# Kernel tuning notes

Hardware: AMD Instinct MI355X
Metric: run time of the kernel (lower is better)

Reference implementation:

```python
import jax, jax.numpy as jnp
import numpy as np

EPS = 1e-5


def setup_inputs() -> dict:
    key = jax.random.key(0)
    k1, k2, k3 = jax.random.split(key, 3)
    B, n_per, C_in, C_out = 8, 131072, 32, 64
    N = B * n_per
    coord = jax.random.uniform(k1, (N, 3), dtype=jnp.float32)          # points in unit cube
    feat = jax.random.normal(k2, (N, C_in), dtype=jnp.float32)
    offset = (jnp.arange(1, B + 1, dtype=jnp.int32) * n_per)           # cumulative counts
    W = jax.random.normal(k3, (C_in, C_out), dtype=jnp.float32) * 0.05  # fc weight (no bias)
    gamma = jnp.ones((C_out,), dtype=jnp.float32)
    beta = jnp.zeros((C_out,), dtype=jnp.float32)
    return {"coord": coord, "feat": feat, "offset": offset, "W": W,
            "gamma": gamma, "beta": beta, "grid_size": 0.05}


def reference(coord, feat, offset, W, gamma, beta, grid_size):
    N = coord.shape[0]
    B = offset.shape[0]
    # offset2batch: point i belongs to batch = first b with i < offset[b]
    batch = jnp.searchsorted(offset, jnp.arange(N, dtype=offset.dtype), side="right").astype(jnp.int32)

    # fc -> BatchNorm (training-mode batch stats, biased var) -> ReLU
    h = feat @ W                                                        # [N, C_out]
    mean = h.mean(axis=0)
    var = jnp.mean((h - mean) ** 2, axis=0)
    h = jax.nn.relu((h - mean) * jax.lax.rsqrt(var + EPS) * gamma + beta)

    # start = per-batch min coord (segment_csr 'min' over batch pointer)
    start = jax.ops.segment_min(coord, batch, num_segments=B)           # [B, 3]

    # voxel_grid: integer voxel coords per point, combined with batch into a unique key
    v = jnp.floor((coord - start[batch]) / grid_size).astype(jnp.int32)  # [N, 3] >= 0
    D = v.max(axis=0) + 1                                               # grid extents
    vkey = ((batch * D[0] + v[:, 0]) * D[1] + v[:, 1]) * D[2] + v[:, 2]

    # unique(sorted) + inverse + counts; then segment mean/max by cluster
    uniq, inverse, counts = jnp.unique(vkey, return_inverse=True, return_counts=True)
    inverse = inverse.reshape(-1).astype(jnp.int32)
    M = uniq.shape[0]
    coord_out = jax.ops.segment_sum(coord, inverse, num_segments=M) / counts[:, None].astype(coord.dtype)
    feat_out = jax.ops.segment_max(h, inverse, num_segments=M)

    # batch id of each cluster (constant within cluster) -> new offset
    batch_out = jax.ops.segment_min(batch, inverse, num_segments=M)
    offset_out = jnp.cumsum(jnp.bincount(batch_out, length=B)).astype(offset.dtype)
    return coord_out, feat_out, offset_out, inverse
```

## Files before the change

kernel.cpp:

```cpp
#include <hip/hip_runtime.h>
#include <float.h>

#define EPSV 1e-5f
#define DGRID 21
#define DPROD (21 * 21 * 21)

typedef __attribute__((ext_vector_type(8))) short bf16x8;
typedef __attribute__((ext_vector_type(4))) float f32x4;

__device__ __forceinline__ short f2bf(float x) {
    unsigned u = __float_as_uint(x);
    unsigned r = (u + 0x7FFFu + ((u >> 16) & 1u)) >> 16;
    return (short)r;
}

__device__ __forceinline__ int batch_of(int i, const int* __restrict__ offset, int B) {
    int b = 0;
    while (b < B - 1 && i >= offset[b]) ++b;
    return b;
}

__global__ void k_init(int* startEnc, int B) {
    int tid = threadIdx.x;
    if (tid < B * 3) startEnc[tid] = 0x7FFFFFFF;
}

__global__ void k_start(const float* __restrict__ coord, const int* __restrict__ offset,
                        int* startEnc, int* counts, int KSM, int N, int B) {
    int gtid = blockIdx.x * blockDim.x + threadIdx.x;
    for (int k = gtid; k < KSM; k += gridDim.x * blockDim.x) counts[k] = 0;

    __shared__ int smin[24];
    int t = threadIdx.x;
    if (t < B * 3) smin[t] = 0x7FFFFFFF;
    __syncthreads();
    int base = gtid * 4;
    int curb = -1;
    int m0 = 0x7FFFFFFF, m1 = 0x7FFFFFFF, m2 = 0x7FFFFFFF;
    for (int r = 0; r < 4; ++r) {
        int i = base + r;
        if (i >= N) break;
        int b = batch_of(i, offset, B);
        if (b != curb) {
            if (curb >= 0) {
                atomicMin(&smin[curb * 3 + 0], m0);
                atomicMin(&smin[curb * 3 + 1], m1);
                atomicMin(&smin[curb * 3 + 2], m2);
            }
            curb = b; m0 = m1 = m2 = 0x7FFFFFFF;
        }
        m0 = min(m0, __float_as_int(coord[(size_t)i * 3 + 0]));
        m1 = min(m1, __float_as_int(coord[(size_t)i * 3 + 1]));
        m2 = min(m2, __float_as_int(coord[(size_t)i * 3 + 2]));
    }
    if (curb >= 0) {
        atomicMin(&smin[curb * 3 + 0], m0);
        atomicMin(&smin[curb * 3 + 1], m1);
        atomicMin(&smin[curb * 3 + 2], m2);
    }
    __syncthreads();
    if (t < B * 3 && smin[t] != 0x7FFFFFFF) atomicMin(&startEnc[t], smin[t]);
}

__global__ void k_count(const float* __restrict__ coord, const int* __restrict__ offset,
                        const int* __restrict__ startEnc, const float* __restrict__ gsP,
                        int* counts, int* vkey, int N, int B) {
    int i = blockIdx.x * blockDim.x + threadIdx.x;
    if (i >= N) return;
    float inv_gs = 1.0f / gsP[0];
    int b = batch_of(i, offset, B);
    float s0 = __int_as_float(startEnc[b * 3 + 0]);
    float s1 = __int_as_float(startEnc[b * 3 + 1]);
    float s2 = __int_as_float(startEnc[b * 3 + 2]);
    int vx = min(DGRID - 1, (int)floorf((coord[(size_t)i * 3 + 0] - s0) * inv_gs));
    int vy = min(DGRID - 1, (int)floorf((coord[(size_t)i * 3 + 1] - s1) * inv_gs));
    int vz = min(DGRID - 1, (int)floorf((coord[(size_t)i * 3 + 2] - s2) * inv_gs));
    int k = ((b * DGRID + vx) * DGRID + vy) * DGRID + vz;
    vkey[i] = k;
    atomicAdd(&counts[k], 1);
}

__global__ void k_scan1(const int* __restrict__ counts, int* occPart, int* cntPart, int KSM) {
    __shared__ int so[256], sc[256];
    int t = threadIdx.x;
    int base = blockIdx.x * 1024 + t * 4;
    int o = 0, c = 0;
    for (int r = 0; r < 4; ++r) {
        int k = base + r;
        if (k < KSM) { int cnt = counts[k]; o += (cnt > 0); c += cnt; }
    }
    so[t] = o; sc[t] = c;
    __syncthreads();
    for (int s = 128; s > 0; s >>= 1) {
        if (t < s) { so[t] += so[t + s]; sc[t] += sc[t + s]; }
        __syncthreads();
    }
    if (t == 0) { occPart[blockIdx.x] = so[0]; cntPart[blockIdx.x] = sc[0]; }
}

__global__ void k_scan2(const int* occPart, const int* cntPart,
                        int* occPartEx, int* cntPartEx, int NBLK) {
    __shared__ int so[128], sc[128];
    int t = threadIdx.x;
    int o = (t < NBLK) ? occPart[t] : 0;
    int c = (t < NBLK) ? cntPart[t] : 0;
    so[t] = o; sc[t] = c;
    __syncthreads();
    for (int s = 1; s < 128; s <<= 1) {
        int ao = 0, ac = 0;
        if (t >= s) { ao = so[t - s]; ac = sc[t - s]; }
        __syncthreads();
        so[t] += ao; sc[t] += ac;
        __syncthreads();
    }
    if (t < NBLK) { occPartEx[t] = so[t] - o; cntPartEx[t] = sc[t] - c; }
}

__global__ void k_scan3(const int* __restrict__ counts, const int* occPartEx, const int* cntPartEx,
                        int* occScan, int* cntScan, int* cursor, int* cntC, int* cstartC, int KSM) {
    __shared__ int so[256], sc[256];
    int t = threadIdx.x;
    int base = blockIdx.x * 1024 + t * 4;
    int o[4], c[4];
    int tO = 0, tC = 0;
    for (int r = 0; r < 4; ++r) {
        int k = base + r;
        int cnt = (k < KSM) ? counts[k] : 0;
        o[r] = (cnt > 0); c[r] = cnt;
        tO += o[r]; tC += c[r];
    }
    so[t] = tO; sc[t] = tC;
    __syncthreads();
    for (int s = 1; s < 256; s <<= 1) {
        int ao = 0, ac = 0;
        if (t >= s) { ao = so[t - s]; ac = sc[t - s]; }
        __syncthreads();
        so[t] += ao; sc[t] += ac;
        __syncthreads();
    }
    int exO = so[t] - tO + occPartEx[blockIdx.x];
    int exC = sc[t] - tC + cntPartEx[blockIdx.x];
    for (int r = 0; r < 4; ++r) {
        int k = base + r;
        if (k < KSM) {
            occScan[k] = exO; cntScan[k] = exC; cursor[k] = 0;
            if (c[r] > 0) { cntC[exO] = c[r]; cstartC[exO] = exC; }
            exO += o[r]; exC += c[r];
        }
    }
}

__global__ void k_scatter(const int* __restrict__ vkey,
                          const int* __restrict__ occScan, const int* __restrict__ cntScan,
                          int* cursor, int* plist, float* __restrict__ dout,
                          int N, int B, int M) {
    int i = blockIdx.x * blockDim.x + threadIdx.x;
    if (i >= N) return;
    int k = vkey[i];
    int cidx = occScan[k];
    int pos = cntScan[k] + atomicAdd(&cursor[k], 1);
    plist[pos] = i;
    dout[(size_t)67 * M + B + i] = (float)cidx;
}

__launch_bounds__(64)
__global__ void k_pool(const float* __restrict__ feat, const float* __restrict__ coord,
                       const float* __restrict__ W,
                       const int* __restrict__ cstartC, const int* __restrict__ cntC,
                       const int* __restrict__ plist,
                       float* __restrict__ dout, float* __restrict__ statPart, int M) {
    const int lane = threadIdx.x;
    const int col  = lane & 15;
    const int quad = lane >> 4;
    const int nw = gridDim.x;
    const int gw = blockIdx.x;

    bf16x8 Bf[4];
#pragma unroll
    for (int t = 0; t < 4; ++t) {
#pragma unroll
        for (int j = 0; j < 8; ++j) {
            int k = quad * 8 + j;
            Bf[t][j] = f2bf(W[k * 64 + t * 16 + col]);
        }
    }

    float sumA[4] = {0.f, 0.f, 0.f, 0.f};
    float sqA[4]  = {0.f, 0.f, 0.f, 0.f};

    for (int c0 = gw; c0 < M; c0 += 2 * nw) {
        int c1 = c0 + nw;
        bool has2 = c1 < M;
        if (!has2) c1 = c0;
        int ps0 = cstartC[c0], n0 = cntC[c0];
        int ps1 = cstartC[c1], n1 = cntC[c1];
        int nmax = max(n0, n1);

        float maxA0[4] = {-FLT_MAX, -FLT_MAX, -FLT_MAX, -FLT_MAX};
        float maxA1[4] = {-FLT_MAX, -FLT_MAX, -FLT_MAX, -FLT_MAX};
        float cacc0 = 0.f, cacc1 = 0.f;

        for (int base = 0; base < nmax; base += 16) {
            int m = base + col;
            int idx0 = min(m, n0 - 1);
            int idx1 = min(m, n1 - 1);
            int p0 = plist[ps0 + idx0];
            int p1 = plist[ps1 + idx1];
            const float4* r0p = reinterpret_cast<const float4*>(feat + (size_t)p0 * 32 + quad * 8);
            const float4* r1p = reinterpret_cast<const float4*>(feat + (size_t)p1 * 32 + quad * 8);
            float4 a00 = r0p[0], a01 = r0p[1];
            float4 a10 = r1p[0], a11 = r1p[1];
            if (quad > 0) {
                float v0 = coord[(size_t)p0 * 3 + (quad - 1)];
                float v1 = coord[(size_t)p1 * 3 + (quad - 1)];
                cacc0 += (m < n0) ? v0 : 0.f;
                cacc1 += (m < n1) ? v1 : 0.f;
            }
            bf16x8 Af0, Af1;
            Af0[0] = f2bf(a00.x); Af0[1] = f2bf(a00.y); Af0[2] = f2bf(a00.z); Af0[3] = f2bf(a00.w);
            Af0[4] = f2bf(a01.x); Af0[5] = f2bf(a01.y); Af0[6] = f2bf(a01.z); Af0[7] = f2bf(a01.w);
            Af1[0] = f2bf(a10.x); Af1[1] = f2bf(a10.y); Af1[2] = f2bf(a10.z); Af1[3] = f2bf(a10.w);
            Af1[4] = f2bf(a11.x); Af1[5] = f2bf(a11.y); Af1[6] = f2bf(a11.z); Af1[7] = f2bf(a11.w);
            f32x4 Cz = {0.f, 0.f, 0.f, 0.f};
#pragma unroll
            for (int t = 0; t < 4; ++t) {
                f32x4 v0 = __builtin_amdgcn_mfma_f32_16x16x32_bf16(Af0, Bf[t], Cz, 0, 0, 0);
                f32x4 v1 = __builtin_amdgcn_mfma_f32_16x16x32_bf16(Af1, Bf[t], Cz, 0, 0, 0);
#pragma unroll
                for (int r = 0; r < 4; ++r) {
                    int rowPt = base + quad * 4 + r;
                    maxA0[t] = fmaxf(maxA0[t], v0[r]);
                    maxA1[t] = fmaxf(maxA1[t], v1[r]);
                    float m0 = (rowPt < n0) ? v0[r] : 0.f;
                    sumA[t] += m0; sqA[t] = fmaf(m0, m0, sqA[t]);
                    float m1 = (rowPt < n1 && has2) ? v1[r] : 0.f;
                    sumA[t] += m1; sqA[t] = fmaf(m1, m1, sqA[t]);
                }
            }
        }
        float out0 = 0.f, out1 = 0.f;
#pragma unroll
        for (int t = 0; t < 4; ++t) {
            float v = maxA0[t];
            v = fmaxf(v, __shfl_xor(v, 16, 64));
            v = fmaxf(v, __shfl_xor(v, 32, 64));
            if (quad == t) out0 = v;
            float w = maxA1[t];
            w = fmaxf(w, __shfl_xor(w, 16, 64));
            w = fmaxf(w, __shfl_xor(w, 32, 64));
            if (quad == t) out1 = w;
        }
        dout[(size_t)3 * M + (size_t)c0 * 64 + lane] = out0;
        dout[(size_t)3 * M + (size_t)c1 * 64 + lane] = out1;

        cacc0 += __shfl_xor(cacc0, 1, 64); cacc0 += __shfl_xor(cacc0, 2, 64);
        cacc0 += __shfl_xor(cacc0, 4, 64); cacc0 += __shfl_xor(cacc0, 8, 64);
        cacc1 += __shfl_xor(cacc1, 1, 64); cacc1 += __shfl_xor(cacc1, 2, 64);
        cacc1 += __shfl_xor(cacc1, 4, 64); cacc1 += __shfl_xor(cacc1, 8, 64);
        if (quad > 0 && col == 0) {
            dout[(size_t)c0 * 3 + (quad - 1)] = cacc0 / (float)n0;
            dout[(size_t)c1 * 3 + (quad - 1)] = cacc1 / (float)n1;
        }
    }

    float so = 0.f, qo = 0.f;
#pragma unroll
    for (int t = 0; t < 4; ++t) {
        float s = sumA[t];
        s += __shfl_xor(s, 16, 64);
        s += __shfl_xor(s, 32, 64);
        float q = sqA[t];
        q += __shfl_xor(q, 16, 64);
        q += __shfl_xor(q, 32, 64);
        if (quad == t) { so = s; qo = q; }
    }
    statPart[(size_t)gw * 128 + lane] = so;
    statPart[(size_t)gw * 128 + 64 + lane] = qo;
}

__global__ void k_statred(const float* __restrict__ statPart,
                          const float* __restrict__ gamma, const float* __restrict__ beta,
                          float* bnA, float* bnB, int NB, int N) {
    __shared__ float s1[256], s2[256];
    int c = blockIdx.x;
    int t = threadIdx.x;
    float a = 0.f, b = 0.f;
    for (int bb = t; bb < NB; bb += 256) {
        a += statPart[(size_t)bb * 128 + c];
        b += statPart[(size_t)bb * 128 + 64 + c];
    }
    s1[t] = a; s2[t] = b;
    __syncthreads();
    for (int s = 128; s > 0; s >>= 1) {
        if (t < s) { s1[t] += s1[t + s]; s2[t] += s2[t + s]; }
        __syncthreads();
    }
    if (t == 0) {
        float invN = 1.0f / (float)N;
        float mean = s1[0] * invN;
        float var = s2[0] * invN - mean * mean;
        float aa = gamma[c] / sqrtf(var + EPSV);
        bnA[c] = aa;
        bnB[c] = beta[c] - mean * aa;
    }
}

__global__ void k_final(float* __restrict__ dout, const float* __restrict__ bnA,
                        const float* __restrict__ bnB,
                        const int* __restrict__ occScan, int M, int B) {
    size_t stride = (size_t)gridDim.x * blockDim.x;
    size_t tid0 = (size_t)blockIdx.x * blockDim.x + threadIdx.x;
    size_t totF = (size_t)M * 64;
    for (size_t t = tid0; t < totF; t += stride) {
        int c = (int)(t & 63);
        float v = dout[(size_t)3 * M + t];
        dout[(size_t)3 * M + t] = fmaxf(bnA[c] * v + bnB[c], 0.f);
    }
    if (tid0 < (size_t)B) {
        int val = (tid0 == (size_t)(B - 1)) ? M : occScan[(int)(tid0 + 1) * DPROD];
        dout[(size_t)67 * M + tid0] = (float)val;
    }
}

extern "C" void kernel_launch(void* const* d_in, const int* in_sizes, int n_in,
                              void* d_out, int out_size, void* d_ws, size_t ws_size,
                              hipStream_t stream) {
    const float* coord = (const float*)d_in[0];
    const float* feat  = (const float*)d_in[1];
    const int*   offset = (const int*)d_in[2];
    const float* W     = (const float*)d_in[3];
    const float* gamma = (const float*)d_in[4];
    const float* beta  = (const float*)d_in[5];
    const float* gsP   = (const float*)d_in[6];
    float* dout = (float*)d_out;

    const int N = in_sizes[0] / 3;
    const int B = in_sizes[2];
    const int M = (out_size - B - N) / 67;
    const int KSM = B * DPROD;
    const int NBLK = (KSM + 1023) / 1024;
    const int NBPL = 8192;

    int* wsI = (int*)d_ws;
    int* startEnc  = wsI + 0;
    float* bnA     = (float*)(wsI + 64);
    float* bnB     = (float*)(wsI + 128);
    int* occPart   = wsI + 256;
    int* cntPart   = wsI + 384;
    int* occPartEx = wsI + 512;
    int* cntPartEx = wsI + 640;
    int* counts    = wsI + 1024;
    int* occScan   = counts + KSM;
    int* cntScan   = occScan + KSM;
    int* cursor    = cntScan + KSM;
    int* cntC      = cursor + KSM;
    int* cstartC   = cntC + KSM;
    int* vkey      = cstartC + KSM;
    int* plist     = vkey + N;
    float* statPart = (float*)(plist + N);

    const int TPB = 256;
    int gChunk = (N + 1023) / 1024;
    int gPoint = (N + TPB - 1) / TPB;

    k_init<<<1, 64, 0, stream>>>(startEnc, B);
    k_start<<<gChunk, TPB, 0, stream>>>(coord, offset, startEnc, counts, KSM, N, B);
    k_count<<<gPoint, TPB, 0, stream>>>(coord, offset, startEnc, gsP, counts, vkey, N, B);
    k_scan1<<<NBLK, TPB, 0, stream>>>(counts, occPart, cntPart, KSM);
    k_scan2<<<1, 128, 0, stream>>>(occPart, cntPart, occPartEx, cntPartEx, NBLK);
    k_scan3<<<NBLK, TPB, 0, stream>>>(counts, occPartEx, cntPartEx, occScan, cntScan,
                                      cursor, cntC, cstartC, KSM);
    k_scatter<<<gPoint, TPB, 0, stream>>>(vkey, occScan, cntScan, cursor, plist,
                                          dout, N, B, M);
    k_pool<<<NBPL, 64, 0, stream>>>(feat, coord, W, cstartC, cntC, plist, dout, statPart, M);
    k_statred<<<64, 256, 0, stream>>>(statPart, gamma, beta, bnA, bnB, NBPL, N);
    k_final<<<1024, TPB, 0, stream>>>(dout, bnA, bnB, occScan, M, B);
}
```

Baseline: 390.3 us.

## Scatter bf16 features and coords into cluster-sorted order for pooling

k_scatter now converts each point's features to bf16 and writes them, along with padded float4 coords, directly into cluster-sorted arrays instead of writing a point index list. k_pool then reads contiguous bf16 rows with no indirection or per-load conversion, and its cluster assignment per block changes to adjacent pairs (2*gw, 2*gw+1). The intent is to replace the random gather in pooling with a single random-write scatter and halve the bytes read there. The cost is extra workspace and scattered 64-byte writes in k_scatter.

```diff
diff --git a/kernel.cpp b/kernel.cpp
--- a/kernel.cpp
+++ b/kernel.cpp
@@ -152,22 +152,40 @@
 
 __global__ void k_scatter(const int* __restrict__ vkey,
                           const int* __restrict__ occScan, const int* __restrict__ cntScan,
-                          int* cursor, int* plist, float* __restrict__ dout,
-                          int N, int B, int M) {
+                          int* cursor,
+                          const float* __restrict__ feat, const float* __restrict__ coord,
+                          short* __restrict__ featR, float* __restrict__ coordR,
+                          float* __restrict__ dout, int N, int B, int M) {
     int i = blockIdx.x * blockDim.x + threadIdx.x;
     if (i >= N) return;
     int k = vkey[i];
     int cidx = occScan[k];
     int pos = cntScan[k] + atomicAdd(&cursor[k], 1);
-    plist[pos] = i;
     dout[(size_t)67 * M + B + i] = (float)cidx;
+
+    const float4* fp = reinterpret_cast<const float4*>(feat + (size_t)i * 32);
+    bf16x8* dst = reinterpret_cast<bf16x8*>(featR + (size_t)pos * 32);
+#pragma unroll
+    for (int t = 0; t < 4; ++t) {
+        float4 a = fp[2 * t];
+        float4 b2 = fp[2 * t + 1];
+        bf16x8 r;
+        r[0] = f2bf(a.x);  r[1] = f2bf(a.y);  r[2] = f2bf(a.z);  r[3] = f2bf(a.w);
+        r[4] = f2bf(b2.x); r[5] = f2bf(b2.y); r[6] = f2bf(b2.z); r[7] = f2bf(b2.w);
+        dst[t] = r;
+    }
+    float4 cv;
+    cv.x = coord[(size_t)i * 3 + 0];
+    cv.y = coord[(size_t)i * 3 + 1];
+    cv.z = coord[(size_t)i * 3 + 2];
+    cv.w = 0.f;
+    *reinterpret_cast<float4*>(coordR + (size_t)pos * 4) = cv;
 }
 
 __launch_bounds__(64)
-__global__ void k_pool(const float* __restrict__ feat, const float* __restrict__ coord,
+__global__ void k_pool(const short* __restrict__ featR, const float* __restrict__ coordR,
                        const float* __restrict__ W,
                        const int* __restrict__ cstartC, const int* __restrict__ cntC,
-                       const int* __restrict__ plist,
                        float* __restrict__ dout, float* __restrict__ statPart, int M) {
     const int lane = threadIdx.x;
     const int col  = lane & 15;
@@ -188,9 +206,9 @@
     float sumA[4] = {0.f, 0.f, 0.f, 0.f};
     float sqA[4]  = {0.f, 0.f, 0.f, 0.f};
 
-    for (int c0 = gw; c0 < M; c0 += 2 * nw) {
-        int c1 = c0 + nw;
-        bool has2 = c1 < M;
+    for (int c0 = 2 * gw; c0 < M; c0 += 2 * nw) {
+        int c1 = c0 + 1;
+        bool has2 = (c1 < M);
         if (!has2) c1 = c0;
         int ps0 = cstartC[c0], n0 = cntC[c0];
         int ps1 = cstartC[c1], n1 = cntC[c1];
@@ -204,23 +222,14 @@
             int m = base + col;
             int idx0 = min(m, n0 - 1);
             int idx1 = min(m, n1 - 1);
-            int p0 = plist[ps0 + idx0];
-            int p1 = plist[ps1 + idx1];
-            const float4* r0p = reinterpret_cast<const float4*>(feat + (size_t)p0 * 32 + quad * 8);
-            const float4* r1p = reinterpret_cast<const float4*>(feat + (size_t)p1 * 32 + quad * 8);
-            float4 a00 = r0p[0], a01 = r0p[1];
-            float4 a10 = r1p[0], a11 = r1p[1];
+            bf16x8 Af0 = *reinterpret_cast<const bf16x8*>(featR + (size_t)(ps0 + idx0) * 32 + quad * 8);
+            bf16x8 Af1 = *reinterpret_cast<const bf16x8*>(featR + (size_t)(ps1 + idx1) * 32 + quad * 8);
             if (quad > 0) {
-                float v0 = coord[(size_t)p0 * 3 + (quad - 1)];
-                float v1 = coord[(size_t)p1 * 3 + (quad - 1)];
+                float v0 = coordR[(size_t)(ps0 + idx0) * 4 + (quad - 1)];
+                float v1 = coordR[(size_t)(ps1 + idx1) * 4 + (quad - 1)];
                 cacc0 += (m < n0) ? v0 : 0.f;
                 cacc1 += (m < n1) ? v1 : 0.f;
             }
-            bf16x8 Af0, Af1;
-            Af0[0] = f2bf(a00.x); Af0[1] = f2bf(a00.y); Af0[2] = f2bf(a00.z); Af0[3] = f2bf(a00.w);
-            Af0[4] = f2bf(a01.x); Af0[5] = f2bf(a01.y); Af0[6] = f2bf(a01.z); Af0[7] = f2bf(a01.w);
-            Af1[0] = f2bf(a10.x); Af1[1] = f2bf(a10.y); Af1[2] = f2bf(a10.z); Af1[3] = f2bf(a10.w);
-            Af1[4] = f2bf(a11.x); Af1[5] = f2bf(a11.y); Af1[6] = f2bf(a11.z); Af1[7] = f2bf(a11.w);
             f32x4 Cz = {0.f, 0.f, 0.f, 0.f};
 #pragma unroll
             for (int t = 0; t < 4; ++t) {
@@ -356,8 +365,9 @@
     int* cntC      = cursor + KSM;
     int* cstartC   = cntC + KSM;
     int* vkey      = cstartC + KSM;
-    int* plist     = vkey + N;
-    float* statPart = (float*)(plist + N);
+    float* statPart = (float*)(vkey + N);
+    short* featR   = (short*)(statPart + (size_t)NBPL * 128);
+    float* coordR  = (float*)(featR + (size_t)N * 32);
 
     const int TPB = 256;
     int gChunk = (N + 1023) / 1024;
@@ -370,9 +380,9 @@
     k_scan2<<<1, 128, 0, stream>>>(occPart, cntPart, occPartEx, cntPartEx, NBLK);
     k_scan3<<<NBLK, TPB, 0, stream>>>(counts, occPartEx, cntPartEx, occScan, cntScan,
                                       cursor, cntC, cstartC, KSM);
-    k_scatter<<<gPoint, TPB, 0, stream>>>(vkey, occScan, cntScan, cursor, plist,
-                                          dout, N, B, M);
-    k_pool<<<NBPL, 64, 0, stream>>>(feat, coord, W, cstartC, cntC, plist, dout, statPart, M);
+    k_scatter<<<gPoint, TPB, 0, stream>>>(vkey, occScan, cntScan, cursor,
+                                          feat, coord, featR, coordR, dout, N, B, M);
+    k_pool<<<NBPL, 64, 0, stream>>>(featR, coordR, W, cstartC, cntC, dout, statPart, M);
     k_statred<<<64, 256, 0, stream>>>(statPart, gamma, beta, bnA, bnB, NBPL, N);
     k_final<<<1024, TPB, 0, stream>>>(dout, bnA, bnB, occScan, M, B);
 }
```

Result: no change. 393.0 us (+0.7%).
